# Kernel optimization log

Measured on AMD Instinct MI355X. Metric: run time of the kernel, lower is better.

## Reference

```python
import jax, jax.numpy as jnp
import numpy as np

SLOPE = 25.0   # fast_sigmoid surrogate slope
BETA = 0.9     # LIF decay
THR = 1.0      # snntorch default threshold
STEPS = 10


@jax.custom_vjp
def spike(x):
    # Heaviside forward, fast-sigmoid surrogate backward
    return (x > 0).astype(x.dtype)

def _spike_fwd(x):
    return spike(x), x

def _spike_bwd(x, g):
    return (g / (SLOPE * jnp.abs(x) + 1.0) ** 2,)

spike.defvjp(_spike_fwd, _spike_bwd)


def lif(inp, mem):
    # snntorch Leaky, reset_mechanism='subtract': reset based on previous mem, detached
    reset = jax.lax.stop_gradient((mem > THR).astype(mem.dtype))
    mem = BETA * mem + inp - reset * THR
    spk = spike(mem - THR)
    return spk, mem


def setup_inputs() -> dict:
    key = jax.random.key(0)
    ks = jax.random.split(key, 4)
    B, IN, H, O = 65536, 512, 1024, 1
    x = jax.random.normal(ks[0], (B, IN), dtype=jnp.float32)
    W1 = jax.random.normal(ks[1], (IN, H), dtype=jnp.float32) / np.sqrt(IN)
    b1 = jnp.zeros((H,), jnp.float32)
    W2 = jax.random.normal(ks[2], (H, H), dtype=jnp.float32) / np.sqrt(H)
    b2 = jnp.zeros((H,), jnp.float32)
    Wo = jax.random.normal(ks[3], (H, O), dtype=jnp.float32) / np.sqrt(H)
    bo = jnp.zeros((O,), jnp.float32)
    return {"x": x, "W1": W1, "b1": b1, "W2": W2, "b2": b2, "Wo": Wo, "bo": bo}


def reference(x, W1, b1, W2, b2, Wo, bo):
    # fc1(x) is identical every timestep (x is static input current)
    cur1 = x @ W1 + b1                      # [B, H]
    B = x.shape[0]
    H = W1.shape[1]
    O = Wo.shape[1]
    m1 = jnp.zeros((B, H), x.dtype)
    m2 = jnp.zeros((B, H), x.dtype)
    mo = jnp.zeros((B, O), x.dtype)

    def step(carry, _):
        m1, m2, mo = carry
        s1, m1 = lif(cur1, m1)
        s2, m2 = lif(s1 @ W2 + b2, m2)
        _, mo = lif(s2 @ Wo + bo, mo)
        return (m1, m2, mo), mo

    _, recs = jax.lax.scan(step, (m1, m2, mo), None, length=STEPS)  # [STEPS, B, O]
    return recs.mean(0)
```

## Files before the change

kernel.cpp:

```cpp
#include <hip/hip_runtime.h>
#include <cstdint>
#include <cstddef>


typedef _Float16 f16;
typedef _Float16 f16x8 __attribute__((ext_vector_type(8)));
typedef float f32x4 __attribute__((ext_vector_type(4)));
typedef int i32x4 __attribute__((ext_vector_type(4)));
typedef unsigned int u32;

#define MFMA16(A, B, C) __builtin_amdgcn_mfma_f32_16x16x32_f16(A, B, C, 0, 0, 0)

static constexpr int BSZ = 65536;
static constexpr int IN = 512;
static constexpr int H = 1024;

__device__ __forceinline__ void gl_lds16(const void* g, void* l) {
    __builtin_amdgcn_global_load_lds(
        (const __attribute__((address_space(1))) u32*)g,
        (__attribute__((address_space(3))) u32*)l, 16, 0, 0);
}

__global__ void prep_dekker(const float* __restrict__ src, f16* __restrict__ dst) {
    int idx = blockIdx.x * 256 + threadIdx.x;
    int k = idx >> 10;
    int j = idx & 1023;
    float w = src[(size_t)k * 1024 + j];
    f16 hi = (f16)w;
    float lo = (w - (float)hi) * 2048.0f;
    size_t o = (size_t)j * 1024 + k;
    dst[o] = hi;
    dst[o + (size_t)H * H] = (f16)lo;
}

__global__ __launch_bounds__(256, 2) void k1_chain(
    const float* __restrict__ x, const float* __restrict__ w1,
    const float* __restrict__ b1, unsigned short* __restrict__ s1b) {
    __shared__ float xs[32][132];
    __shared__ float ws[32][256];
    const int hblk = blockIdx.x;
    const int bblk = blockIdx.y;
    const int tid = threadIdx.x;
    const int ht = tid & 15, bt = tid >> 4;
    const int h0 = hblk * 256, b0 = bblk * 128;

    float acc[8][16] = {};

    float4 xv[4], wv[8];
#pragma unroll
    for (int i = 0; i < 4; ++i) {
        int idx = tid + 256 * i;
        int br = idx >> 3, ks = idx & 7;
        xv[i] = *(const float4*)&x[(size_t)(b0 + br) * IN + ks * 4];
    }
#pragma unroll
    for (int i = 0; i < 8; ++i) {
        int idx = tid + 256 * i;
        int kr = idx >> 6, c4 = idx & 63;
        wv[i] = *(const float4*)&w1[(size_t)kr * H + h0 + c4 * 4];
    }

    for (int kc = 0; kc < 512; kc += 32) {
        __syncthreads();
#pragma unroll
        for (int i = 0; i < 4; ++i) {
            int idx = tid + 256 * i;
            int br = idx >> 3, ks = idx & 7;
            xs[ks * 4 + 0][br] = xv[i].x;
            xs[ks * 4 + 1][br] = xv[i].y;
            xs[ks * 4 + 2][br] = xv[i].z;
            xs[ks * 4 + 3][br] = xv[i].w;
        }
#pragma unroll
        for (int i = 0; i < 8; ++i) {
            int idx = tid + 256 * i;
            int kr = idx >> 6, c4 = idx & 63;
            *(float4*)&ws[kr][c4 * 4] = wv[i];
        }
        __syncthreads();
        int kn = (kc + 32) & 511;
#pragma unroll
        for (int i = 0; i < 4; ++i) {
            int idx = tid + 256 * i;
            int br = idx >> 3, ks = idx & 7;
            xv[i] = *(const float4*)&x[(size_t)(b0 + br) * IN + kn + ks * 4];
        }
#pragma unroll
        for (int i = 0; i < 8; ++i) {
            int idx = tid + 256 * i;
            int kr = idx >> 6, c4 = idx & 63;
            wv[i] = *(const float4*)&w1[(size_t)(kn + kr) * H + h0 + c4 * 4];
        }
#pragma unroll 2
        for (int k = 0; k < 32; ++k) {
            float xr[8];
            *(float4*)&xr[0] = *(const float4*)&xs[k][bt * 8];
            *(float4*)&xr[4] = *(const float4*)&xs[k][bt * 8 + 4];
            float wr[16];
#pragma unroll
            for (int g = 0; g < 4; ++g)
                *(float4*)&wr[g * 4] = *(const float4*)&ws[k][ht * 4 + 64 * g];
#pragma unroll
            for (int i = 0; i < 8; ++i)
#pragma unroll
                for (int j = 0; j < 16; ++j)
                    acc[i][j] = fmaf(xr[i], wr[j], acc[i][j]);
        }
    }

    float b1v[16];
#pragma unroll
    for (int g = 0; g < 4; ++g)
#pragma unroll
        for (int m = 0; m < 4; ++m)
            b1v[g * 4 + m] = b1[h0 + g * 64 + ht * 4 + m];
#pragma unroll
    for (int i = 0; i < 8; ++i) {
        unsigned short outb[16];
#pragma unroll
        for (int j = 0; j < 16; ++j) {
            float c = __fadd_rn(acc[i][j], b1v[j]);
            float m = 0.0f;
            unsigned bits = 0u;
#pragma unroll
            for (int t = 0; t < 10; ++t) {
                float rst = (m > 1.0f) ? 1.0f : 0.0f;
                m = __fmul_rn(0.9f, m);
                m = __fadd_rn(m, c);
                m = __fsub_rn(m, rst);
                if (m > 1.0f) bits |= (1u << t);
            }
            outb[j] = (unsigned short)bits;
        }
        size_t row = (size_t)(b0 + bt * 8 + i);
#pragma unroll
        for (int g = 0; g < 4; ++g)
            *(int2*)&s1b[row * H + h0 + g * 64 + ht * 4] = ((const int2*)outb)[g];
    }
}

__global__ __launch_bounds__(512, 4) void k2_spikes_gemm(
    const unsigned short* __restrict__ s1bits, const f16* __restrict__ w2d,
    const float* __restrict__ b2, u32* __restrict__ po32) {
    __shared__ __align__(16) char ldsraw[32768];
    i32x4 (*AL)[2][4][64]    = (i32x4 (*)[2][4][64])ldsraw;
    i32x4 (*BL)[2][2][2][64] = (i32x4 (*)[2][2][2][64])(ldsraw + 16384);

    const int jblk = blockIdx.x, bblk = blockIdx.y;
    const int tid = threadIdx.x;
    const int lane = tid & 63, wave = tid >> 6;
    const int strip = wave & 3, cfw = wave >> 2;
    const int l15 = lane & 15, loct = lane >> 4;

    const bool stB = (wave >= 4);
    const int bp = (wave >> 1) & 1, bcf = wave & 1;
    const unsigned short* gA =
        s1bits + (size_t)(bblk * 64 + strip * 16 + l15) * 1024 + loct * 8;
    const f16* gB = w2d + (size_t)bp * H * H
                  + (size_t)(jblk * 32 + bcf * 16 + l15) * 1024 + loct * 8;

    f32x4 acc[10][2] = {};

    typedef union { i32x4 i; unsigned long long u[2]; f16x8 h; } U;

#define STAGE(t_)                                                        \
    do {                                                                 \
        int bi_ = (t_) & 1;                                              \
        int kk_ = ((t_) * 64) & 1023;                                    \
        if (stB) {                                                       \
            gl_lds16(gB + kk_,      &BL[bi_][0][bp][bcf][0]);            \
            gl_lds16(gB + kk_ + 32, &BL[bi_][1][bp][bcf][0]);            \
        } else {                                                         \
            gl_lds16(gA + kk_,      &AL[bi_][0][strip][0]);              \
            gl_lds16(gA + kk_ + 32, &AL[bi_][1][strip][0]);              \
        }                                                                \
    } while (0)

    STAGE(0);
    asm volatile("s_waitcnt vmcnt(0)" ::: "memory");
    __builtin_amdgcn_s_barrier();

    for (int t = 0; t < 16; ++t) {
        const int bi = t & 1;
        STAGE(t + 1);
#pragma unroll
        for (int kch = 0; kch < 2; ++kch) {
            U m;
            m.i = AL[bi][kch][strip][lane];
            U b0v; b0v.i = BL[bi][kch][0][cfw][lane];
            U b1v; b1v.i = BL[bi][kch][1][cfw][lane];
            f16x8 bf0 = b0v.h, bf1 = b1v.h;
            __builtin_amdgcn_s_setprio(1);
#pragma unroll
            for (int tt = 0; tt < 10; ++tt) {
                const int sh = 10 - tt;
                U r;
                r.u[0] = (m.u[0] << sh) & 0x0400040004000400ULL;
                r.u[1] = (m.u[1] << sh) & 0x0400040004000400ULL;
                acc[tt][0] = MFMA16(r.h, bf0, acc[tt][0]);
                acc[tt][1] = MFMA16(r.h, bf1, acc[tt][1]);
            }
            __builtin_amdgcn_s_setprio(0);
        }
        asm volatile("s_waitcnt vmcnt(0)" ::: "memory");
        __builtin_amdgcn_s_barrier();
    }
#undef STAGE

    int col0 = jblk * 32 + cfw * 16 + l15;
    float b2v = b2[col0];
    float m2[4] = {0.0f, 0.0f, 0.0f, 0.0f};
    unsigned short* pw = (unsigned short*)po32;

#pragma unroll
    for (int tt = 0; tt < 10; ++tt) {
#pragma unroll
        for (int r = 0; r < 4; ++r) {
            float iv = (float)((double)acc[tt][0][r] * 16384.0 + (double)acc[tt][1][r] * 8.0);
            iv = __fadd_rn(iv, b2v);
            float rst = (m2[r] > 1.0f) ? 1.0f : 0.0f;
            m2[r] = __fmul_rn(0.9f, m2[r]);
            m2[r] = __fadd_rn(m2[r], iv);
            m2[r] = __fsub_rn(m2[r], rst);
            unsigned long long bal = __ballot(m2[r] > 1.0f);
            if (l15 == r) {
                int row = bblk * 64 + strip * 16 + loct * 4 + r;
                pw[(((size_t)jblk * 10 + tt) * BSZ + row) * 2 + cfw] =
                    (unsigned short)(bal >> (loct * 16));
            }
        }
    }
}

__global__ __launch_bounds__(256) void k3_out(
    const u32* __restrict__ po32, const float* __restrict__ wo,
    const float* __restrict__ bo, float* __restrict__ out) {
    __shared__ float wos[1024];
    const int tid = threadIdx.x;
    for (int i = tid; i < 1024; i += 256) wos[i] = wo[i];
    __syncthreads();
    const int b = blockIdx.x * 256 + tid;

    float inp[10] = {};
    for (int jb = 0; jb < 32; ++jb) {
        float wr[32];
#pragma unroll
        for (int g = 0; g < 8; ++g)
            *(float4*)&wr[g * 4] = *(const float4*)&wos[jb * 32 + g * 4];
#pragma unroll
        for (int t = 0; t < 10; ++t) {
            u32 mk = po32[((size_t)jb * 10 + t) * BSZ + b];
#pragma unroll
            for (int bit = 0; bit < 32; ++bit)
                inp[t] += ((mk >> bit) & 1u) ? wr[bit] : 0.0f;
        }
    }

    float bov = bo[0];
    float mo = 0.0f, s = 0.0f;
#pragma unroll
    for (int t = 0; t < 10; ++t) {
        float iv = __fadd_rn(inp[t], bov);
        float rst = (mo > 1.0f) ? 1.0f : 0.0f;
        mo = __fmul_rn(0.9f, mo);
        mo = __fadd_rn(mo, iv);
        mo = __fsub_rn(mo, rst);
        s += mo;
    }
    out[b] = s / 10.0f;
}

extern "C" void kernel_launch(void* const* d_in, const int* in_sizes, int n_in,
                              void* d_out, int out_size, void* d_ws, size_t ws_size,
                              hipStream_t stream) {
    (void)in_sizes; (void)n_in; (void)out_size; (void)ws_size;
    const float* x  = (const float*)d_in[0];
    const float* W1 = (const float*)d_in[1];
    const float* b1 = (const float*)d_in[2];
    const float* W2 = (const float*)d_in[3];
    const float* b2 = (const float*)d_in[4];
    const float* Wo = (const float*)d_in[5];
    const float* bo = (const float*)d_in[6];
    float* out = (float*)d_out;

    char* ws = (char*)d_ws;
    f16* w2d = (f16*)ws;
    unsigned short* s1bits = (unsigned short*)(ws + ((size_t)16 << 20));
    u32* po32 = (u32*)(ws + ((size_t)160 << 20));

    prep_dekker<<<dim3((H * H) / 256), 256, 0, stream>>>(W2, w2d);
    k1_chain<<<dim3(4, BSZ / 128), 256, 0, stream>>>(x, W1, b1, s1bits);
    k2_spikes_gemm<<<dim3(H / 32, BSZ / 64), 512, 0, stream>>>(s1bits, w2d, b2, po32);
    k3_out<<<dim3(BSZ / 256), 256, 0, stream>>>(po32, Wo, bo, out);
}
```

Baseline: 3.403 ms.

## Replace LDS-staged operand loads with direct register-prefetched global loads in k2

Removes the shared-memory double buffer and the global_load_lds staging in the spike GEMM. Each wave now loads its own A and B fragments straight from global memory into registers and prefetches the next k-chunk one iteration ahead. This drops the per-iteration barriers and LDS traffic. The cost is duplicated global/L2 reads, since A is reloaded by both column waves and B by all four strip waves, plus higher register pressure, which is why launch bounds drop from 4 to 2 blocks per CU.

```diff
diff --git a/kernel.cpp b/kernel.cpp
--- a/kernel.cpp
+++ b/kernel.cpp
@@ -14,12 +14,6 @@
 static constexpr int BSZ = 65536;
 static constexpr int IN = 512;
 static constexpr int H = 1024;
-
-__device__ __forceinline__ void gl_lds16(const void* g, void* l) {
-    __builtin_amdgcn_global_load_lds(
-        (const __attribute__((address_space(1))) u32*)g,
-        (__attribute__((address_space(3))) u32*)l, 16, 0, 0);
-}
 
 __global__ void prep_dekker(const float* __restrict__ src, f16* __restrict__ dst) {
     int idx = blockIdx.x * 256 + threadIdx.x;
@@ -139,57 +133,45 @@
     }
 }
 
-__global__ __launch_bounds__(512, 4) void k2_spikes_gemm(
+__global__ __launch_bounds__(512, 2) void k2_spikes_gemm(
     const unsigned short* __restrict__ s1bits, const f16* __restrict__ w2d,
     const float* __restrict__ b2, u32* __restrict__ po32) {
-    __shared__ __align__(16) char ldsraw[32768];
-    i32x4 (*AL)[2][4][64]    = (i32x4 (*)[2][4][64])ldsraw;
-    i32x4 (*BL)[2][2][2][64] = (i32x4 (*)[2][2][2][64])(ldsraw + 16384);
-
     const int jblk = blockIdx.x, bblk = blockIdx.y;
     const int tid = threadIdx.x;
     const int lane = tid & 63, wave = tid >> 6;
     const int strip = wave & 3, cfw = wave >> 2;
     const int l15 = lane & 15, loct = lane >> 4;
 
-    const bool stB = (wave >= 4);
-    const int bp = (wave >> 1) & 1, bcf = wave & 1;
     const unsigned short* gA =
         s1bits + (size_t)(bblk * 64 + strip * 16 + l15) * 1024 + loct * 8;
-    const f16* gB = w2d + (size_t)bp * H * H
-                  + (size_t)(jblk * 32 + bcf * 16 + l15) * 1024 + loct * 8;
+    const f16* gB0 = w2d + (size_t)(jblk * 32 + cfw * 16 + l15) * 1024 + loct * 8;
+    const f16* gB1 = gB0 + (size_t)H * H;
 
     f32x4 acc[10][2] = {};
 
     typedef union { i32x4 i; unsigned long long u[2]; f16x8 h; } U;
 
-#define STAGE(t_)                                                        \
-    do {                                                                 \
-        int bi_ = (t_) & 1;                                              \
-        int kk_ = ((t_) * 64) & 1023;                                    \
-        if (stB) {                                                       \
-            gl_lds16(gB + kk_,      &BL[bi_][0][bp][bcf][0]);            \
-            gl_lds16(gB + kk_ + 32, &BL[bi_][1][bp][bcf][0]);            \
-        } else {                                                         \
-            gl_lds16(gA + kk_,      &AL[bi_][0][strip][0]);              \
-            gl_lds16(gA + kk_ + 32, &AL[bi_][1][strip][0]);              \
-        }                                                                \
-    } while (0)
-
-    STAGE(0);
-    asm volatile("s_waitcnt vmcnt(0)" ::: "memory");
-    __builtin_amdgcn_s_barrier();
-
+    i32x4 a0c = *(const i32x4*)(gA);
+    i32x4 a1c = *(const i32x4*)(gA + 32);
+    i32x4 b00c = *(const i32x4*)(gB0);
+    i32x4 b01c = *(const i32x4*)(gB0 + 32);
+    i32x4 b10c = *(const i32x4*)(gB1);
+    i32x4 b11c = *(const i32x4*)(gB1 + 32);
+
+#pragma unroll 2
     for (int t = 0; t < 16; ++t) {
-        const int bi = t & 1;
-        STAGE(t + 1);
-#pragma unroll
-        for (int kch = 0; kch < 2; ++kch) {
-            U m;
-            m.i = AL[bi][kch][strip][lane];
-            U b0v; b0v.i = BL[bi][kch][0][cfw][lane];
-            U b1v; b1v.i = BL[bi][kch][1][cfw][lane];
-            f16x8 bf0 = b0v.h, bf1 = b1v.h;
+        const int kn = ((t + 1) * 64) & 1023;
+        i32x4 a0n = *(const i32x4*)(gA + kn);
+        i32x4 a1n = *(const i32x4*)(gA + kn + 32);
+        i32x4 b00n = *(const i32x4*)(gB0 + kn);
+        i32x4 b01n = *(const i32x4*)(gB0 + kn + 32);
+        i32x4 b10n = *(const i32x4*)(gB1 + kn);
+        i32x4 b11n = *(const i32x4*)(gB1 + kn + 32);
+        {
+            U m; m.i = a0c;
+            U p0; p0.i = b00c;
+            U p1; p1.i = b10c;
+            f16x8 bf0 = p0.h, bf1 = p1.h;
             __builtin_amdgcn_s_setprio(1);
 #pragma unroll
             for (int tt = 0; tt < 10; ++tt) {
@@ -202,10 +184,26 @@
             }
             __builtin_amdgcn_s_setprio(0);
         }
-        asm volatile("s_waitcnt vmcnt(0)" ::: "memory");
-        __builtin_amdgcn_s_barrier();
-    }
-#undef STAGE
+        {
+            U m; m.i = a1c;
+            U p0; p0.i = b01c;
+            U p1; p1.i = b11c;
+            f16x8 bf0 = p0.h, bf1 = p1.h;
+            __builtin_amdgcn_s_setprio(1);
+#pragma unroll
+            for (int tt = 0; tt < 10; ++tt) {
+                const int sh = 10 - tt;
+                U r;
+                r.u[0] = (m.u[0] << sh) & 0x0400040004000400ULL;
+                r.u[1] = (m.u[1] << sh) & 0x0400040004000400ULL;
+                acc[tt][0] = MFMA16(r.h, bf0, acc[tt][0]);
+                acc[tt][1] = MFMA16(r.h, bf1, acc[tt][1]);
+            }
+            __builtin_amdgcn_s_setprio(0);
+        }
+        a0c = a0n; a1c = a1n;
+        b00c = b00n; b01c = b01n; b10c = b10n; b11c = b11n;
+    }
 
     int col0 = jblk * 32 + cfw * 16 + l15;
     float b2v = b2[col0];
```

New measurement: 4.481 ms. 1.32x slower.
